# Performance work log

Hardware: AMD Instinct MI355X
Metric: run time of the kernel (lower is better)

## Reference

```python
import jax, jax.numpy as jnp
import numpy as np

B, I, O, H = 1024, 64, 64, 32  # batch, input_size, output_size, hidden_size
NEG_SLOPE = 0.01  # nn.LeakyReLU default


def leaky(x):
    return jnp.where(x >= 0, x, NEG_SLOPE * x)


def setup_inputs() -> dict:
    key = jax.random.key(0)
    ks = jax.random.split(key, 9)
    u = lambda k, shape, b: jax.random.uniform(k, shape, jnp.float32, -b, b)
    # Per-edge tiny MLP params, stacked over [O, I] edges.
    # Linear(1,H): fan_in=1 -> bound 1.0 ; Linear(H,H)/Linear(H,1): bound 1/sqrt(H)
    bnd = 1.0 / np.sqrt(H)
    return {
        "x": jax.random.normal(ks[0], (B, I), jnp.float32),
        "W1": u(ks[1], (O, I, H), 1.0),        # Linear(1,H) weight
        "b1": u(ks[2], (O, I, H), 1.0),
        "W2": u(ks[3], (O, I, H, H), bnd),     # Linear(H,H) weight [out,in]
        "b2": u(ks[4], (O, I, H), bnd),
        "W3": u(ks[5], (O, I, H), bnd),        # Linear(H,1) weight
        "b3": u(ks[6], (O, I), bnd),
        "layer_w": jnp.ones((O, I), jnp.float32),           # layer_weight init 1.0
        "bias_w": u(ks[7], (O, I), 0.1),                     # bias_weight ~ U(-0.1,0.1)
    }


def reference(x, W1, b1, W2, b2, W3, b3, layer_w, bias_w):
    # All O*I edge MLPs evaluated as one batched computation.
    # h1[b,o,i,h] = leaky(x[b,i] * W1[o,i,h] + b1[o,i,h])
    h1 = leaky(x[:, None, :, None] * W1 + b1)                      # [B,O,I,H]
    h2 = leaky(jnp.einsum('boih,oikh->boik', h1, W2) + b2)         # [B,O,I,H]
    edge = jnp.einsum('boih,oih->boi', h2, W3) + b3                # [B,O,I]
    edge = bias_w * leaky(x)[:, None, :] + layer_w * edge          # per-edge output
    return edge.sum(axis=2)                                        # [B,O]
```

## Files before the change

### kernel.cpp

```cpp
#include <hip/hip_runtime.h>


#define H_   32
#define NI   64
#define NO   64
#define NB   1024
#define ROWS 128
#define MT   8
#define XSTR 66
#define NWAVE 4

typedef float    floatx4 __attribute__((ext_vector_type(4)));
typedef _Float16 halfx8  __attribute__((ext_vector_type(8)));
typedef _Float16 halfx2  __attribute__((ext_vector_type(2)));

union H8 { halfx8 v8; halfx2 v2[4]; unsigned int u[4]; };

__device__ inline float leaky(float v) { return fmaxf(v, 0.01f * v); }

__device__ inline unsigned int pkrtz(float a, float b) {
    return __builtin_bit_cast(unsigned int, __builtin_amdgcn_cvt_pkrtz(a, b));
}

__global__ __launch_bounds__(256, 4)
void kan_kernel(const float* __restrict__ x,  const float* __restrict__ W1,
                const float* __restrict__ b1, const float* __restrict__ W2,
                const float* __restrict__ b2, const float* __restrict__ W3,
                const float* __restrict__ b3, const float* __restrict__ lw,
                const float* __restrict__ bw, float* __restrict__ out)
{
    __shared__ unsigned int xsp[ROWS * XSTR];
    __shared__ _Float16 w1s[NI * H_];
    __shared__ _Float16 b1s[NI * H_];
    __shared__ unsigned int wbs[NI * H_];
    __shared__ float rc[ROWS];
    __shared__ float part[NWAVE][ROWS];

    const int t    = threadIdx.x;
    const int o    = blockIdx.x;
    const int row0 = blockIdx.y * ROWS;

    const float* xsrc = x + (size_t)row0 * NI;
    #pragma unroll
    for (int v = 0; v < 8; ++v) {
        int fe = (v * 256 + t) * 4;
        int r = fe >> 6, c = fe & 63;
        float4 xv = *(const float4*)(xsrc + fe);
        uint2 lo = { pkrtz(xv.x, xv.x), pkrtz(xv.y, xv.y) };
        uint2 hi = { pkrtz(xv.z, xv.z), pkrtz(xv.w, xv.w) };
        *(uint2*)(&xsp[r * XSTR + c])     = lo;
        *(uint2*)(&xsp[r * XSTR + c + 2]) = hi;
    }
    const float* w1g = W1 + (size_t)o * NI * H_;
    const float* b1g = b1 + (size_t)o * NI * H_;
    #pragma unroll
    for (int v = 0; v < 2; ++v) {
        int e = (v * 256 + t) * 4;
        float4 a = *(const float4*)(w1g + e);
        float4 c = *(const float4*)(b1g + e);
        uint2 pa = { pkrtz(a.x, a.y), pkrtz(a.z, a.w) };
        uint2 pc = { pkrtz(c.x, c.y), pkrtz(c.z, c.w) };
        *(uint2*)(w1s + e) = pa;
        *(uint2*)(b1s + e) = pc;
    }
    {
        int e = t * 8;
        float l = lw[o * NI + (e >> 5)];
        const float* w3g = W3 + (size_t)o * NI * H_ + e;
        const float* b2g = b2 + (size_t)o * NI * H_ + e;
        float4 wa = *(const float4*)(w3g), wb = *(const float4*)(w3g + 4);
        float4 ba = *(const float4*)(b2g), bb = *(const float4*)(b2g + 4);
        uint4 p0 = { pkrtz(l * wa.x, ba.x), pkrtz(l * wa.y, ba.y),
                     pkrtz(l * wa.z, ba.z), pkrtz(l * wa.w, ba.w) };
        uint4 p1 = { pkrtz(l * wb.x, bb.x), pkrtz(l * wb.y, bb.y),
                     pkrtz(l * wb.z, bb.z), pkrtz(l * wb.w, bb.w) };
        *(uint4*)(&wbs[e])     = p0;
        *(uint4*)(&wbs[e + 4]) = p1;
    }
    __syncthreads();

    const int lane = t & 63, wave = t >> 6;
    const int col  = lane & 15;
    const int kh   = lane >> 4;
    const int koff = kh * 8;
    const int i0   = wave * 16;

    const float* w2p0 = W2 + ((size_t)(o * NI + i0) * H_ + col) * H_ + koff;
    const float* w2p1 = w2p0 + 16 * H_;
    const halfx2 slope = { (_Float16)0.01f, (_Float16)0.01f };

    floatx4 pacc[MT];
    #pragma unroll
    for (int m = 0; m < MT; ++m)
        pacc[m] = floatx4{0.f, 0.f, 0.f, 0.f};

    floatx4 a0 = *(const floatx4*)(w2p0);
    floatx4 a1 = *(const floatx4*)(w2p0 + 4);
    floatx4 a2 = *(const floatx4*)(w2p1);
    floatx4 a3 = *(const floatx4*)(w2p1 + 4);

    #pragma unroll 2
    for (int ii = 0; ii < 16; ++ii) {
        const int i = i0 + ii;

        floatx4 n0, n1, n2, n3;
        if (ii < 15) {
            const float* np0 = w2p0 + (ii + 1) * (H_ * H_);
            const float* np1 = w2p1 + (ii + 1) * (H_ * H_);
            n0 = *(const floatx4*)(np0);
            n1 = *(const floatx4*)(np0 + 4);
            n2 = *(const floatx4*)(np1);
            n3 = *(const floatx4*)(np1 + 4);
        }

        H8 bf0, bf1;
        bf0.u[0] = pkrtz(a0[0], a0[1]);  bf0.u[1] = pkrtz(a0[2], a0[3]);
        bf0.u[2] = pkrtz(a1[0], a1[1]);  bf0.u[3] = pkrtz(a1[2], a1[3]);
        bf1.u[0] = pkrtz(a2[0], a2[1]);  bf1.u[1] = pkrtz(a2[2], a2[3]);
        bf1.u[2] = pkrtz(a3[0], a3[1]);  bf1.u[3] = pkrtz(a3[2], a3[3]);

        H8 w1v, b1v;
        w1v.v8 = *(const halfx8*)(w1s + i * H_ + koff);
        b1v.v8 = *(const halfx8*)(b1s + i * H_ + koff);

        halfx2 q0 = __builtin_bit_cast(halfx2, wbs[i * H_ + col]);
        halfx2 q1 = __builtin_bit_cast(halfx2, wbs[i * H_ + col + 16]);
        float w3e0 = (float)q0[0], b2c0 = (float)q0[1];
        float w3e1 = (float)q1[0], b2c1 = (float)q1[1];
        float p0 = 0.505f * w3e0, nn0 = 0.495f * w3e0;
        float p1 = 0.505f * w3e1, nn1 = 0.495f * w3e1;

        #pragma unroll
        for (int m = 0; m < MT; ++m) {
            halfx2 xx = __builtin_bit_cast(halfx2, xsp[(m * 16 + col) * XSTR + i]);
            H8 af;
            #pragma unroll
            for (int j = 0; j < 4; ++j) {
                halfx2 h = __builtin_elementwise_fma(xx, w1v.v2[j], b1v.v2[j]);
                af.v2[j] = __builtin_elementwise_max(h, h * slope);
            }
            floatx4 c0 = { b2c0, b2c0, b2c0, b2c0 };
            floatx4 c1 = { b2c1, b2c1, b2c1, b2c1 };
            c0 = __builtin_amdgcn_mfma_f32_16x16x32_f16(af.v8, bf0.v8, c0, 0, 0, 0);
            c1 = __builtin_amdgcn_mfma_f32_16x16x32_f16(af.v8, bf1.v8, c1, 0, 0, 0);
            #pragma unroll
            for (int r = 0; r < 4; ++r) {
                float acc = pacc[m][r];
                acc = fmaf(p0,  c0[r],
                      fmaf(nn0, fabsf(c0[r]),
                      fmaf(p1,  c1[r],
                      fmaf(nn1, fabsf(c1[r]), acc))));
                pacc[m][r] = acc;
            }
        }

        a0 = n0; a1 = n1; a2 = n2; a3 = n3;
    }

    #pragma unroll
    for (int m = 0; m < MT; ++m) {
        #pragma unroll
        for (int r = 0; r < 4; ++r) {
            float v = pacc[m][r];
            v += __shfl_xor(v, 1, 64);
            v += __shfl_xor(v, 2, 64);
            v += __shfl_xor(v, 4, 64);
            v += __shfl_xor(v, 8, 64);
            if (col == 0)
                part[wave][m * 16 + kh * 4 + r] = v;
        }
    }

    if (t < ROWS) {
        float s = 0.f;
        const float* bwp = bw + o * NI;
        const float* lp  = lw + o * NI;
        const float* b3p = b3 + o * NI;
        for (int i = 0; i < NI; ++i) {
            halfx2 hx = __builtin_bit_cast(halfx2, xsp[t * XSTR + i]);
            s += bwp[i] * leaky((float)hx[0]) + lp[i] * b3p[i];
        }
        rc[t] = s;
    }
    __syncthreads();

    if (t < ROWS) {
        float v = rc[t];
        #pragma unroll
        for (int w = 0; w < NWAVE; ++w) v += part[w][t];
        out[(size_t)(row0 + t) * NO + o] = v;
    }
}

extern "C" void kernel_launch(void* const* d_in, const int* in_sizes, int n_in,
                              void* d_out, int out_size, void* d_ws, size_t ws_size,
                              hipStream_t stream) {
    const float* x  = (const float*)d_in[0];
    const float* W1 = (const float*)d_in[1];
    const float* b1 = (const float*)d_in[2];
    const float* W2 = (const float*)d_in[3];
    const float* b2 = (const float*)d_in[4];
    const float* W3 = (const float*)d_in[5];
    const float* b3 = (const float*)d_in[6];
    const float* lw = (const float*)d_in[7];
    const float* bw = (const float*)d_in[8];
    float* out = (float*)d_out;

    dim3 grid(NO, NB / ROWS);
    kan_kernel<<<grid, dim3(256), 0, stream>>>(x, W1, b1, W2, b2, W3, b3, lw, bw, out);
}
```

Baseline: 111.2 us.

## Halve rows per block and deepen W2 register prefetch to two stages

Each block now processes 64 batch rows instead of 128, doubling the grid to 1024 blocks. The W2 prefetch is now two iterations deep, using rotating register sets with a clamped index instead of a conditional single-step load. More blocks should improve load balance and latency hiding across CUs. The cost is that each W2 slice is re-read by twice as many blocks, increasing global and L2 traffic, and the deeper pipeline uses more registers.

Measured after the change: 112.5 us. Within noise of the previous version (+1.2%).

```diff
diff --git a/kernel.cpp b/kernel.cpp
--- a/kernel.cpp
+++ b/kernel.cpp
@@ -5,8 +5,8 @@
 #define NI   64
 #define NO   64
 #define NB   1024
-#define ROWS 128
-#define MT   8
+#define ROWS 64
+#define MT   4
 #define XSTR 66
 #define NWAVE 4
 
@@ -42,7 +42,7 @@
 
     const float* xsrc = x + (size_t)row0 * NI;
     #pragma unroll
-    for (int v = 0; v < 8; ++v) {
+    for (int v = 0; v < 4; ++v) {
         int fe = (v * 256 + t) * 4;
         int r = fe >> 6, c = fe & 63;
         float4 xv = *(const float4*)(xsrc + fe);
@@ -94,30 +94,33 @@
     for (int m = 0; m < MT; ++m)
         pacc[m] = floatx4{0.f, 0.f, 0.f, 0.f};
 
-    floatx4 a0 = *(const floatx4*)(w2p0);
-    floatx4 a1 = *(const floatx4*)(w2p0 + 4);
-    floatx4 a2 = *(const floatx4*)(w2p1);
-    floatx4 a3 = *(const floatx4*)(w2p1 + 4);
-
-    #pragma unroll 2
+    floatx4 A0, A1, A2, A3;
+    floatx4 B0, B1, B2, B3;
+    A0 = *(const floatx4*)(w2p0);
+    A1 = *(const floatx4*)(w2p0 + 4);
+    A2 = *(const floatx4*)(w2p1);
+    A3 = *(const floatx4*)(w2p1 + 4);
+    B0 = *(const floatx4*)(w2p0 + 1024);
+    B1 = *(const floatx4*)(w2p0 + 1028);
+    B2 = *(const floatx4*)(w2p1 + 1024);
+    B3 = *(const floatx4*)(w2p1 + 1028);
+
     for (int ii = 0; ii < 16; ++ii) {
         const int i = i0 + ii;
 
-        floatx4 n0, n1, n2, n3;
-        if (ii < 15) {
-            const float* np0 = w2p0 + (ii + 1) * (H_ * H_);
-            const float* np1 = w2p1 + (ii + 1) * (H_ * H_);
-            n0 = *(const floatx4*)(np0);
-            n1 = *(const floatx4*)(np0 + 4);
-            n2 = *(const floatx4*)(np1);
-            n3 = *(const floatx4*)(np1 + 4);
-        }
+        int ip = ii + 2; ip = (ip > 15) ? 15 : ip;
+        const float* np0 = w2p0 + ip * 1024;
+        const float* np1 = w2p1 + ip * 1024;
+        floatx4 C0 = *(const floatx4*)(np0);
+        floatx4 C1 = *(const floatx4*)(np0 + 4);
+        floatx4 C2 = *(const floatx4*)(np1);
+        floatx4 C3 = *(const floatx4*)(np1 + 4);
 
         H8 bf0, bf1;
-        bf0.u[0] = pkrtz(a0[0], a0[1]);  bf0.u[1] = pkrtz(a0[2], a0[3]);
-        bf0.u[2] = pkrtz(a1[0], a1[1]);  bf0.u[3] = pkrtz(a1[2], a1[3]);
-        bf1.u[0] = pkrtz(a2[0], a2[1]);  bf1.u[1] = pkrtz(a2[2], a2[3]);
-        bf1.u[2] = pkrtz(a3[0], a3[1]);  bf1.u[3] = pkrtz(a3[2], a3[3]);
+        bf0.u[0] = pkrtz(A0[0], A0[1]);  bf0.u[1] = pkrtz(A0[2], A0[3]);
+        bf0.u[2] = pkrtz(A1[0], A1[1]);  bf0.u[3] = pkrtz(A1[2], A1[3]);
+        bf1.u[0] = pkrtz(A2[0], A2[1]);  bf1.u[1] = pkrtz(A2[2], A2[3]);
+        bf1.u[2] = pkrtz(A3[0], A3[1]);  bf1.u[3] = pkrtz(A3[2], A3[3]);
 
         H8 w1v, b1v;
         w1v.v8 = *(const halfx8*)(w1s + i * H_ + koff);
@@ -154,7 +157,8 @@
             }
         }
 
-        a0 = n0; a1 = n1; a2 = n2; a3 = n3;
+        A0 = B0; A1 = B1; A2 = B2; A3 = B3;
+        B0 = C0; B1 = C1; B2 = C2; B3 = C3;
     }
 
     #pragma unroll
```
